# Optimization experiments

Measured on AMD Instinct MI355X. Metric: run time of the kernel, lower is better.

Reference implementation:

```python
import jax, jax.numpy as jnp
import numpy as np

INPUT_SIZE = 64
HIDDEN_SIZE = 128
LATENT_B = 8
BATCH = 512
SEQ = 2048


def setup_inputs() -> dict:
    key = jax.random.key(0)
    ks = jax.random.split(key, 8)
    s_fc = 1.0 / np.sqrt(INPUT_SIZE)
    s_gru = 1.0 / np.sqrt(LATENT_B)
    return {
        "latent_A_seq": jax.random.normal(ks[0], (BATCH, SEQ, INPUT_SIZE), dtype=jnp.float32),
        # fc_in: Linear(input_size -> hidden_size)
        "W_in": jax.random.uniform(ks[1], (HIDDEN_SIZE, INPUT_SIZE), jnp.float32, -s_fc, s_fc),
        "b_in": jax.random.uniform(ks[2], (HIDDEN_SIZE,), jnp.float32, -s_fc, s_fc),
        # GRU(hidden_size -> latent_dim_B), PyTorch layout: [3*H, in] stacked as (r, z, n)
        "W_ih": jax.random.uniform(ks[3], (3 * LATENT_B, HIDDEN_SIZE), jnp.float32, -s_gru, s_gru),
        "W_hh": jax.random.uniform(ks[4], (3 * LATENT_B, LATENT_B), jnp.float32, -s_gru, s_gru),
        "b_ih": jax.random.uniform(ks[5], (3 * LATENT_B,), jnp.float32, -s_gru, s_gru),
        "b_hh": jax.random.uniform(ks[6], (3 * LATENT_B,), jnp.float32, -s_gru, s_gru),
    }


def reference(latent_A_seq, W_in, b_in, W_ih, W_hh, b_ih, b_hh):
    # fc_in projection: (B, S, input) -> (B, S, hidden)
    x = jnp.einsum("bsi,hi->bsh", latent_A_seq, W_in) + b_in
    H = W_hh.shape[1]

    # Precompute input-side gate activations for all timesteps: (B, S, 3H)
    x_gates = jnp.einsum("bsh,gh->bsg", x, W_ih) + b_ih
    xr, xz, xn = jnp.split(x_gates, 3, axis=-1)

    Whr, Whz, Whn = jnp.split(W_hh, 3, axis=0)
    bhr, bhz, bhn = jnp.split(b_hh, 3, axis=0)

    def step(h, gates_t):
        xr_t, xz_t, xn_t = gates_t
        r = jax.nn.sigmoid(xr_t + h @ Whr.T + bhr)
        z = jax.nn.sigmoid(xz_t + h @ Whz.T + bhz)
        n = jnp.tanh(xn_t + r * (h @ Whn.T + bhn))
        h_new = (1.0 - z) * n + z * h
        return h_new, None

    h0 = jnp.zeros((latent_A_seq.shape[0], H), dtype=latent_A_seq.dtype)
    # scan over time: move seq axis to front -> (S, B, H) per gate
    seq_gates = (jnp.swapaxes(xr, 0, 1), jnp.swapaxes(xz, 0, 1), jnp.swapaxes(xn, 0, 1))
    h_final, _ = jax.lax.scan(step, h0, seq_gates)
    return h_final  # (B, latent_dim_B) == h_n.squeeze(0)
```

## Files before the change

kernel.cpp:

```cpp
#include <hip/hip_runtime.h>
#include <math.h>

#define BATCH  512
#define SEQ    2048
#define INPUT  64
#define HID    128
#define LB     8
#define NG     24
#define T      16
#define NCHUNK (SEQ / T)
#define BPB    2
#define RPC    (BPB * T)
#define RSTR   28

#define LOG2E  1.44269504088896340736f

typedef float v2f __attribute__((ext_vector_type(2)));
__device__ __forceinline__ v2f mk2(float a, float b) { v2f r; r.x = a; r.y = b; return r; }

#if __has_builtin(__builtin_amdgcn_exp2f)
#define EXP2F(x) __builtin_amdgcn_exp2f(x)
#else
#define EXP2F(x) __expf(0.69314718055994530942f * (x))
#endif

__global__ void precompute_kernel(const float* __restrict__ W_in,
                                  const float* __restrict__ b_in,
                                  const float* __restrict__ W_ih,
                                  const float* __restrict__ b_ih,
                                  const float* __restrict__ b_hh,
                                  float* __restrict__ Wc,
                                  float* __restrict__ bc)
{
    int t = blockIdx.x * blockDim.x + threadIdx.x;
    if (t < NG * INPUT) {
        int g = t / INPUT, i = t % INPUT;
        float acc = 0.f;
        for (int h = 0; h < HID; ++h)
            acc += W_ih[g * HID + h] * W_in[h * INPUT + i];
        float sc = (g < 2 * LB) ? -LOG2E : 2.0f * LOG2E;
        Wc[t] = acc * sc;
    } else if (t < NG * INPUT + NG) {
        int g = t - NG * INPUT;
        float acc = b_ih[g];
        if (g < 2 * LB) acc += b_hh[g];
        for (int h = 0; h < HID; ++h)
            acc += W_ih[g * HID + h] * b_in[h];
        float sc = (g < 2 * LB) ? -LOG2E : 2.0f * LOG2E;
        bc[g] = acc * sc;
    }
}

#define ROR2(v)  __int_as_float(__builtin_amdgcn_update_dpp(0, __float_as_int(v), 0x122, 0xF, 0xF, false))
#define ROR4(v)  __int_as_float(__builtin_amdgcn_update_dpp(0, __float_as_int(v), 0x124, 0xF, 0xF, false))
#define ROR8(v)  __int_as_float(__builtin_amdgcn_update_dpp(0, __float_as_int(v), 0x128, 0xF, 0xF, false))
#define SWAP1(v) __int_as_float(__builtin_amdgcn_update_dpp(0, __float_as_int(v), 0x0B1, 0xF, 0xF, false))

#define GATHER8(sl, x) do {      \
    sl[0] = (x);                 \
    sl[1] = ROR2(sl[0]);         \
    sl[2] = ROR4(sl[0]);         \
    sl[3] = ROR4(sl[1]);         \
    sl[4] = ROR8(sl[0]);         \
    sl[5] = ROR8(sl[1]);         \
    sl[6] = ROR8(sl[2]);         \
    sl[7] = ROR8(sl[3]);         \
} while (0)

__device__ __forceinline__ void prod_round(
    int c, int r, int h,
    const float* __restrict__ arow,
    const float4* __restrict__ wl,
    float* __restrict__ sbuf,
    float4 (&cur)[8], float4 (&nxt)[8])
{
    if (c + 1 < NCHUNK) {
        const float* src = arow + (size_t)(c + 1) * (T * INPUT);
#pragma unroll
        for (int i = 0; i < 8; ++i)
            nxt[i] = *(const float4*)(src + i * 4);
    }

    v2f acc[NG];
#pragma unroll
    for (int g = 0; g < NG; ++g) acc[g] = mk2(0.f, 0.f);
#pragma unroll
    for (int g = 0; g < NG; ++g) {
#pragma unroll
        for (int i = 0; i < 8; ++i) {
            float4 w = wl[g * 16 + i];
            float4 a = cur[i];
            acc[g] += mk2(a.x, a.y) * mk2(w.x, w.y)
                    + mk2(a.z, a.w) * mk2(w.z, w.w);
        }
    }

    float s[NG];
#pragma unroll
    for (int g = 0; g < NG; ++g) {
        float v = acc[g].x + acc[g].y;
        s[g] = v + SWAP1(v);
    }

    if (h == 0) {
        float4* dst = (float4*)(sbuf + (c & 1) * (RPC * RSTR) + r * RSTR);
#pragma unroll
        for (int q = 0; q < 6; ++q)
            dst[q] = make_float4(s[4 * q], s[4 * q + 1], s[4 * q + 2], s[4 * q + 3]);
    }
    __syncthreads();
}

__global__ __launch_bounds__(128, 1) void fused_kernel(
    const float* __restrict__ A,
    const float* __restrict__ Wc,
    const float* __restrict__ bc,
    const float* __restrict__ W_hh,
    const float* __restrict__ b_hh,
    float* __restrict__ out)
{
    __shared__ float  sbuf[2 * RPC * RSTR];
    __shared__ float4 wlds4[NG * 16];

    const int tid = threadIdx.x;
    const int wv  = tid >> 6;
    const int l   = tid & 63;
    const int b0  = blockIdx.x * BPB;

    {
        const float4* Wc4 = (const float4*)Wc;
        for (int idx = tid; idx < NG * 16; idx += 128)
            wlds4[idx] = Wc4[idx];
    }

    if (wv == 0) {
        const int r = l >> 1;
        const int h = l & 1;
        const float* arow = A + ((size_t)(b0 + (r >> 4)) * SEQ + (r & 15)) * INPUT
                              + h * 32;
        const float4* wl = wlds4 + h * 8;

        float4 a0[8], a1[8];
#pragma unroll
        for (int i = 0; i < 8; ++i)
            a0[i] = *(const float4*)(arow + i * 4);

        __syncthreads();

        prod_round(0, r, h, arow, wl, sbuf, a0, a1);
        for (int p = 1; p < NCHUNK - 1; p += 2) {
            prod_round(p,     r, h, arow, wl, sbuf, a1, a0);
            prod_round(p + 1, r, h, arow, wl, sbuf, a0, a1);
        }
        prod_round(NCHUNK - 1, r, h, arow, wl, sbuf, a1, a0);
    } else {
        const int row = l >> 4;
        const int j   = (l >> 1) & 7;
        const int g   = l & 1;
        const int bh  = row * 2 + g;
        const int bhc = bh & (BPB - 1);

        float jdxv[8];
        GATHER8(jdxv, (float)j);
        float wrs[8], wzs[8], wns[8];
#pragma unroll
        for (int m = 0; m < 8; ++m) {
            int idx = (int)(jdxv[m] + 0.5f);
            wrs[m] = W_hh[(0 * LB + j) * LB + idx] * (-LOG2E);
            wzs[m] = W_hh[(1 * LB + j) * LB + idx] * (-LOG2E);
            wns[m] = W_hh[(2 * LB + j) * LB + idx] * (2.0f * LOG2E);
        }
        v2f wr2[4], wz2[4], wn2[4];
#pragma unroll
        for (int m = 0; m < 4; ++m) {
            wr2[m] = mk2(wrs[2 * m], wrs[2 * m + 1]);
            wz2[m] = mk2(wzs[2 * m], wzs[2 * m + 1]);
            wn2[m] = mk2(wns[2 * m], wns[2 * m + 1]);
        }
        const float bxr = bc[j];
        const float bxz = bc[8 + j];
        const float bxn = bc[16 + j];
        const float bhn = b_hh[2 * LB + j] * (2.0f * LOG2E);

        float hreg = 0.f;
        __syncthreads();
        __syncthreads();

        for (int p = 0; p < NCHUNK; ++p) {
            const float* Lb = sbuf + (p & 1) * (RPC * RSTR) + bhc * (T * RSTR) + j;

            float cr = Lb[0]  + bxr, cz = Lb[8]  + bxz, cn = Lb[16] + bxn;
            float nr = Lb[RSTR] + bxr, nz = Lb[RSTR + 8] + bxz, nn = Lb[RSTR + 16] + bxn;
#pragma unroll
            for (int d = 0; d < T; ++d) {
                float fr = 0.f, fz = 0.f, fn = 0.f;
                if (d + 2 < T) {
                    const float* q = Lb + (d + 2) * RSTR;
                    fr = q[0] + bxr; fz = q[8] + bxz; fn = q[16] + bxn;
                }

                float hs[8];
                GATHER8(hs, hreg);
                v2f h0 = mk2(hs[0], hs[1]);
                v2f h1 = mk2(hs[2], hs[3]);
                v2f h2 = mk2(hs[4], hs[5]);
                v2f h3 = mk2(hs[6], hs[7]);

                v2f srv = h0 * wr2[0] + h1 * wr2[1] + (h2 * wr2[2] + h3 * wr2[3]);
                v2f szv = h0 * wz2[0] + h1 * wz2[1] + (h2 * wz2[2] + h3 * wz2[3]);
                v2f snv = h0 * wn2[0] + h1 * wn2[1] + (h2 * wn2[2] + h3 * wn2[3]);

                float dr = cr + (srv.x + srv.y);
                float dz = cz + (szv.x + szv.y);
                float dn = bhn + (snv.x + snv.y);

                float er = EXP2F(dr);
                float ez = EXP2F(dz);
                float rr = __builtin_amdgcn_rcpf(1.f + er);
                float zz = __builtin_amdgcn_rcpf(1.f + ez);

                float tt = fmaf(rr, dn, cn);
                float en = EXP2F(tt);
                float nv = fmaf(-2.f, __builtin_amdgcn_rcpf(1.f + en), 1.f);

                hreg = fmaf(zz, hreg - nv, nv);

                cr = nr; cz = nz; cn = nn;
                nr = fr; nz = fz; nn = fn;
            }
            if (p + 1 < NCHUNK) __syncthreads();
        }

        if (bh < BPB)
            out[(b0 + bh) * LB + j] = hreg;
    }
}

extern "C" void kernel_launch(void* const* d_in, const int* in_sizes, int n_in,
                              void* d_out, int out_size, void* d_ws, size_t ws_size,
                              hipStream_t stream) {
    const float* A    = (const float*)d_in[0];
    const float* W_in = (const float*)d_in[1];
    const float* b_in = (const float*)d_in[2];
    const float* W_ih = (const float*)d_in[3];
    const float* W_hh = (const float*)d_in[4];
    const float* b_ih = (const float*)d_in[5];
    const float* b_hh = (const float*)d_in[6];
    float* out = (float*)d_out;

    float* Wc = (float*)d_ws;
    float* bc = Wc + NG * INPUT;

    precompute_kernel<<<7, 256, 0, stream>>>(W_in, b_in, W_ih, b_ih, b_hh, Wc, bc);
    fused_kernel<<<BATCH / BPB, 128, 0, stream>>>(A, Wc, bc, W_hh, b_hh, out);
}
```

Measured before the change: 816.7 us.

## Split the gate-projection producer across two wavefronts, each handling twelve gates

The block grows from 128 to 192 threads, so two producer wavefronts each compute half of the 24 input-gate projections per chunk and write their halves into the shared staging buffer. The recurrent consumer moves to the third wavefront. The producer loop is also rewritten to stream weights from LDS in a three-deep rotating register buffer, with sched_barrier calls to control instruction ordering. This aims to shorten the per-chunk producer time that the serial consumer waits on. It adds a wave per block, and it swaps the prefetch buffers through runtime pointers, which may push those register arrays to scratch memory.

After: 1.408 ms. 72.4% more time.

```diff
diff --git a/kernel.cpp b/kernel.cpp
--- a/kernel.cpp
+++ b/kernel.cpp
@@ -12,6 +12,7 @@
 #define BPB    2
 #define RPC    (BPB * T)
 #define RSTR   28
+#define GPW    12
 
 #define LOG2E  1.44269504088896340736f
 
@@ -67,51 +68,7 @@
     sl[7] = ROR8(sl[3]);         \
 } while (0)
 
-__device__ __forceinline__ void prod_round(
-    int c, int r, int h,
-    const float* __restrict__ arow,
-    const float4* __restrict__ wl,
-    float* __restrict__ sbuf,
-    float4 (&cur)[8], float4 (&nxt)[8])
-{
-    if (c + 1 < NCHUNK) {
-        const float* src = arow + (size_t)(c + 1) * (T * INPUT);
-#pragma unroll
-        for (int i = 0; i < 8; ++i)
-            nxt[i] = *(const float4*)(src + i * 4);
-    }
-
-    v2f acc[NG];
-#pragma unroll
-    for (int g = 0; g < NG; ++g) acc[g] = mk2(0.f, 0.f);
-#pragma unroll
-    for (int g = 0; g < NG; ++g) {
-#pragma unroll
-        for (int i = 0; i < 8; ++i) {
-            float4 w = wl[g * 16 + i];
-            float4 a = cur[i];
-            acc[g] += mk2(a.x, a.y) * mk2(w.x, w.y)
-                    + mk2(a.z, a.w) * mk2(w.z, w.w);
-        }
-    }
-
-    float s[NG];
-#pragma unroll
-    for (int g = 0; g < NG; ++g) {
-        float v = acc[g].x + acc[g].y;
-        s[g] = v + SWAP1(v);
-    }
-
-    if (h == 0) {
-        float4* dst = (float4*)(sbuf + (c & 1) * (RPC * RSTR) + r * RSTR);
-#pragma unroll
-        for (int q = 0; q < 6; ++q)
-            dst[q] = make_float4(s[4 * q], s[4 * q + 1], s[4 * q + 2], s[4 * q + 3]);
-    }
-    __syncthreads();
-}
-
-__global__ __launch_bounds__(128, 1) void fused_kernel(
+__global__ __launch_bounds__(192, 1) void fused_kernel(
     const float* __restrict__ A,
     const float* __restrict__ Wc,
     const float* __restrict__ bc,
@@ -129,16 +86,16 @@
 
     {
         const float4* Wc4 = (const float4*)Wc;
-        for (int idx = tid; idx < NG * 16; idx += 128)
+        for (int idx = tid; idx < NG * 16; idx += 192)
             wlds4[idx] = Wc4[idx];
     }
 
-    if (wv == 0) {
+    if (wv < 2) {
         const int r = l >> 1;
         const int h = l & 1;
         const float* arow = A + ((size_t)(b0 + (r >> 4)) * SEQ + (r & 15)) * INPUT
                               + h * 32;
-        const float4* wl = wlds4 + h * 8;
+        const float4* wl = wlds4 + (wv * GPW) * 16 + h * 8;
 
         float4 a0[8], a1[8];
 #pragma unroll
@@ -147,12 +104,56 @@
 
         __syncthreads();
 
-        prod_round(0, r, h, arow, wl, sbuf, a0, a1);
-        for (int p = 1; p < NCHUNK - 1; p += 2) {
-            prod_round(p,     r, h, arow, wl, sbuf, a1, a0);
-            prod_round(p + 1, r, h, arow, wl, sbuf, a0, a1);
-        }
-        prod_round(NCHUNK - 1, r, h, arow, wl, sbuf, a1, a0);
+        float4* cur = a0;
+        float4* nxt = a1;
+        for (int c = 0; c < NCHUNK; ++c) {
+            if (c + 1 < NCHUNK) {
+                const float* src = arow + (size_t)(c + 1) * (T * INPUT);
+#pragma unroll
+                for (int i = 0; i < 8; ++i)
+                    nxt[i] = *(const float4*)(src + i * 4);
+            }
+            __builtin_amdgcn_sched_barrier(0);
+
+            float4 wb[3][8];
+#pragma unroll
+            for (int i = 0; i < 8; ++i) wb[0][i] = wl[0 * 16 + i];
+#pragma unroll
+            for (int i = 0; i < 8; ++i) wb[1][i] = wl[1 * 16 + i];
+            __builtin_amdgcn_sched_barrier(0);
+
+            float s[GPW];
+#pragma unroll
+            for (int g = 0; g < GPW; ++g) {
+                if (g + 2 < GPW) {
+#pragma unroll
+                    for (int i = 0; i < 8; ++i)
+                        wb[(g + 2) % 3][i] = wl[(g + 2) * 16 + i];
+                }
+                __builtin_amdgcn_sched_barrier(0);
+                v2f acc = mk2(0.f, 0.f);
+#pragma unroll
+                for (int i = 0; i < 8; ++i) {
+                    float4 w = wb[g % 3][i];
+                    float4 a = cur[i];
+                    acc += mk2(a.x, a.y) * mk2(w.x, w.y)
+                         + mk2(a.z, a.w) * mk2(w.z, w.w);
+                }
+                float v = acc.x + acc.y;
+                s[g] = v + SWAP1(v);
+            }
+
+            if (h == 0) {
+                float* dst = sbuf + (c & 1) * (RPC * RSTR) + r * RSTR + wv * GPW;
+#pragma unroll
+                for (int q = 0; q < 3; ++q)
+                    ((float4*)dst)[q] = make_float4(s[4 * q], s[4 * q + 1],
+                                                    s[4 * q + 2], s[4 * q + 3]);
+            }
+            __syncthreads();
+
+            float4* t = cur; cur = nxt; nxt = t;
+        }
     } else {
         const int row = l >> 4;
         const int j   = (l >> 1) & 7;
@@ -252,5 +253,5 @@
     float* bc = Wc + NG * INPUT;
 
     precompute_kernel<<<7, 256, 0, stream>>>(W_in, b_in, W_ih, b_ih, b_hh, Wc, bc);
-    fused_kernel<<<BATCH / BPB, 128, 0, stream>>>(A, Wc, bc, W_hh, b_hh, out);
+    fused_kernel<<<BATCH / BPB, 192, 0, stream>>>(A, Wc, bc, W_hh, b_hh, out);
 }
```
